# Kernel tuning notes

Hardware: AMD Instinct MI355X
Metric: run time of the kernel (lower is better)

Reference implementation:

```python
import jax, jax.numpy as jnp
import numpy as np

B, T, D, H, DFF = 64, 100, 1024, 16, 4096
HD = D // H
EPS = 1e-5


def _rope_tables(t_len, hd, dtype):
    # matches RotaryEmbedding: inv_freq over even dims, emb = cat([freqs, freqs])
    inv_freq = 1.0 / (10000.0 ** (jnp.arange(0, hd, 2, dtype=jnp.float32) / hd))
    t = jnp.arange(t_len, dtype=jnp.float32)
    freqs = jnp.einsum('i,j->ij', t, inv_freq)          # (T, hd/2)
    emb = jnp.concatenate([freqs, freqs], axis=-1)      # (T, hd)
    # apply_rope uses cos[..., ::2] / sin[..., ::2]
    cos = jnp.cos(emb)[:, ::2].astype(dtype)            # (T, hd/2)
    sin = jnp.sin(emb)[:, ::2].astype(dtype)
    return cos, sin


def _apply_rope(x, cos, sin):
    # x: (B, H, T, hd); cos/sin: (T, hd/2) broadcast over B,H
    x1 = x[..., ::2]
    x2 = x[..., 1::2]
    return jnp.concatenate([x1 * cos - x2 * sin, x1 * sin + x2 * cos], axis=-1)


def _layernorm(x, g, b):
    mu = jnp.mean(x, axis=-1, keepdims=True)
    var = jnp.mean(jnp.square(x - mu), axis=-1, keepdims=True)
    return (x - mu) * jax.lax.rsqrt(var + EPS) * g + b


def setup_inputs() -> dict:
    key = jax.random.key(0)
    ks = jax.random.split(key, 8)
    s = 0.02
    return {
        'tgt': jax.random.normal(ks[0], (B, T, D), dtype=jnp.float32),
        'Wqkv': jax.random.normal(ks[1], (3 * D, D), dtype=jnp.float32) * s,
        'bqkv': jnp.zeros((3 * D,), jnp.float32),
        'Wo': jax.random.normal(ks[2], (D, D), dtype=jnp.float32) * s,
        'bo': jnp.zeros((D,), jnp.float32),
        'W1': jax.random.normal(ks[3], (DFF, D), dtype=jnp.float32) * s,
        'b1': jnp.zeros((DFF,), jnp.float32),
        'W2': jax.random.normal(ks[4], (D, DFF), dtype=jnp.float32) * s,
        'b2': jnp.zeros((D,), jnp.float32),
        'g1': jnp.ones((D,), jnp.float32),
        'be1': jnp.zeros((D,), jnp.float32),
        'g2': jnp.ones((D,), jnp.float32),
        'be2': jnp.zeros((D,), jnp.float32),
        'tgt_mask': jnp.tril(jnp.ones((T, T), jnp.int32)),
    }


def reference(tgt, Wqkv, bqkv, Wo, bo, W1, b1, W2, b2, g1, be1, g2, be2, tgt_mask):
    dtype = tgt.dtype
    # QKV projection (torch Linear: x @ W.T + b)
    qkv = jnp.einsum('btd,ed->bte', tgt, Wqkv) + bqkv          # (B,T,3D)
    qkv = qkv.reshape(B, T, 3, H, HD).transpose(2, 0, 3, 1, 4)  # (3,B,H,T,hd)
    q, k, v = qkv[0], qkv[1], qkv[2]

    cos, sin = _rope_tables(T, HD, dtype)
    q = _apply_rope(q, cos, sin)
    k = _apply_rope(k, cos, sin)

    scale = 1.0 / np.sqrt(HD)
    scores = jnp.einsum('bhqd,bhkd->bhqk', q, k) * scale        # (B,H,T,T)
    scores = jnp.where(tgt_mask == 0, -jnp.inf, scores)
    attn = jax.nn.softmax(scores, axis=-1)
    ctx = jnp.einsum('bhqk,bhkd->bhqd', attn, v)                # (B,H,T,hd)
    ctx = ctx.transpose(0, 2, 1, 3).reshape(B, T, D)

    tgt2 = jnp.einsum('btd,ed->bte', ctx, Wo) + bo
    x = _layernorm(tgt + tgt2, g1, be1)

    h = jax.nn.relu(jnp.einsum('btd,fd->btf', x, W1) + b1)
    ff = jnp.einsum('btf,df->btd', h, W2) + b2
    out = _layernorm(x + ff, g2, be2)
    return out
```

## Files before the change

### kernel.cpp

```cpp
#include <hip/hip_runtime.h>
#include <math.h>

#define Bn   64
#define Tn   100
#define Tp   128
#define Dn   1024
#define Hn   16
#define HDn  64
#define DFFn 4096
#define EPSf 1e-5f

typedef unsigned short ushort_t;
typedef __attribute__((ext_vector_type(8))) __bf16 bf16x8;
typedef __attribute__((ext_vector_type(4))) float f32x4;

__device__ __forceinline__ float u2f(ushort_t u) {
    union { unsigned int i; float f; } v; v.i = ((unsigned int)u) << 16; return v.f;
}
__device__ __forceinline__ ushort_t f2bf(float f) {
    union { float f; unsigned int u; } v; v.f = f;
    unsigned int r = v.u + 0x7FFFu + ((v.u >> 16) & 1u);
    return (ushort_t)(r >> 16);
}

__device__ __forceinline__ void gload_lds16(const void* g, void* l) {
    __builtin_amdgcn_global_load_lds(
        (const __attribute__((address_space(1))) unsigned int*)g,
        (__attribute__((address_space(3))) unsigned int*)l,
        16, 0, 0);
}

#define VMWAIT_(n) asm volatile("s_waitcnt vmcnt(" #n ")" ::: "memory")
#define VMWAIT(n)  VMWAIT_(n)

struct ConvSeg { const float* src; ushort_t* dst; int n4; };
struct Conv5   { ConvSeg seg[5]; };

__global__ __launch_bounds__(256) void conv_bf16_multi(Conv5 cfg)
{
    int i = blockIdx.x * 256 + threadIdx.x;
    #pragma unroll
    for (int s = 0; s < 5; ++s) {
        const int n = cfg.seg[s].n4;
        if (i < n) {
            float4 v = ((const float4*)cfg.seg[s].src)[i];
            ushort4 o;
            o.x = f2bf(v.x); o.y = f2bf(v.y); o.z = f2bf(v.z); o.w = f2bf(v.w);
            ((ushort4*)cfg.seg[s].dst)[i] = o;
            return;
        }
        i -= n;
    }
}

#define GEMM_TILE_MAP(gx_, gy_, swz_)                                        \
    const int L  = blockIdx.x;                                               \
    int rowt, colt;                                                          \
    if (swz_) {                                                              \
        const int group = L / (8 * (gx_));                                   \
        int l = L - group * 8 * (gx_);                                       \
        const int rem = (gy_) - group * 8;                                   \
        if (rem >= 8) { rowt = group * 8 + (l & 7); colt = l >> 3; }         \
        else          { rowt = group * 8 + l % rem; colt = l / rem; }        \
    } else { rowt = L / (gx_); colt = L - rowt * (gx_); }

#define GEMM_KLOOP(A_, B_, K_)                                               \
    for (int k0 = 0; k0 < (K_); k0 += 64) {                                  \
        __syncthreads();                                                     \
        _Pragma("unroll")                                                    \
        for (int t = 0; t < 4; ++t) {                                        \
            const int idx = (wave * 4 + t) * 64 + lane;                      \
            const int row = idx >> 3;                                        \
            const int gc  = (idx & 7) ^ (row & 7);                           \
            gload_lds16((A_) + (size_t)(row0 + row) * (K_) + k0 + gc * 8,    \
                        &As[idx * 8]);                                       \
            gload_lds16((B_) + (size_t)(col0 + row) * (K_) + k0 + gc * 8,    \
                        &Bs[idx * 8]);                                       \
        }                                                                    \
        __syncthreads();                                                     \
        _Pragma("unroll")                                                    \
        for (int kh = 0; kh < 2; ++kh) {                                     \
            const int chunk = kh * 4 + g;                                    \
            bf16x8 af[4], bfr[4];                                            \
            _Pragma("unroll")                                                \
            for (int i = 0; i < 4; ++i) {                                    \
                const int ra = wrow + i * 16 + frow;                         \
                af[i]  = *(const bf16x8*)&As[ra * 64 + (chunk ^ (ra & 7)) * 8]; \
                const int rb = wcol + i * 16 + frow;                         \
                bfr[i] = *(const bf16x8*)&Bs[rb * 64 + (chunk ^ (rb & 7)) * 8]; \
            }                                                                \
            _Pragma("unroll")                                                \
            for (int i = 0; i < 4; ++i)                                      \
                _Pragma("unroll")                                            \
                for (int j = 0; j < 4; ++j)                                  \
                    acc[i][j] = __builtin_amdgcn_mfma_f32_16x16x32_bf16(     \
                        af[i], bfr[j], acc[i][j], 0, 0, 0);                  \
        }                                                                    \
    }

template<int BN, bool RELU, bool ADDRES, typename OutT>
__global__ __launch_bounds__(512, 2) void gemm256_bt(const ushort_t* __restrict__ A,
                                                     const ushort_t* __restrict__ Bm,
                                                     const float* __restrict__ bias,
                                                     const ushort_t* __restrict__ res,
                                                     OutT* __restrict__ C,
                                                     int M, int N, int K,
                                                     int gx, int swz)
{
    constexpr int JN = BN / 64;
    constexpr int NB = BN / 128;
    __shared__ __align__(16) ushort_t As[2][256 * 64];
    __shared__ __align__(16) ushort_t Bs[2][BN * 64];

    const int gy = M >> 8;
    GEMM_TILE_MAP(gx, gy, swz)

    const int tid  = threadIdx.x;
    const int lane = tid & 63;
    const int wave = tid >> 6;
    const int wm   = wave >> 2;
    const int wn   = wave & 3;
    const int row0 = rowt * 256;
    const int col0 = colt * BN;
    const int frow = lane & 15;
    const int g    = lane >> 4;

    auto stageA = [&](const ushort_t* src, int rowbase, ushort_t* lds) {
        #pragma unroll
        for (int i = 0; i < 2; ++i) {
            const int idx = i * 512 + tid;
            const int row = idx >> 3;
            const int gc  = (idx & 7) ^ (row & 7);
            gload_lds16(src + (size_t)(rowbase + row) * K + gc * 8, lds + idx * 8);
        }
    };
    auto stageB = [&](const ushort_t* src, int rowbase, ushort_t* lds) {
        #pragma unroll
        for (int i = 0; i < NB; ++i) {
            const int idx = i * 512 + tid;
            const int row = idx >> 3;
            const int gc  = (idx & 7) ^ (row & 7);
            gload_lds16(src + (size_t)(rowbase + row) * K + gc * 8, lds + idx * 8);
        }
    };

    f32x4 acc[8][JN] = {};

    const int NT = K >> 6;
    stageB(Bm,      col0,          &Bs[0][0]);
    stageB(Bm,      col0 + BN / 2, &Bs[0][(BN / 2) * 64]);
    stageA(A,       row0,          &As[0][0]);
    stageA(A,       row0 + 128,    &As[0][128 * 64]);
    stageB(Bm + 64, col0,          &Bs[1][0]);
    stageB(Bm + 64, col0 + BN / 2, &Bs[1][(BN / 2) * 64]);
    if constexpr (NB == 2) { VMWAIT(4); } else { VMWAIT(2); }
    __builtin_amdgcn_s_barrier();

    for (int t = 0; t < NT; ++t) {
        const int  buf = t & 1;
        const bool stA = (t + 1 < NT);
        const bool stB = (t + 2 < NT);

        if constexpr (BN == 128) {
            bf16x8 bfr[JN][2];
            #pragma unroll
            for (int j = 0; j < JN; ++j)
                #pragma unroll
                for (int kk = 0; kk < 2; ++kk) {
                    const int rb = wn * (BN / 4) + j * 16 + frow;
                    const int ch = kk * 4 + g;
                    bfr[j][kk] = *(const bf16x8*)&Bs[buf][rb * 64 + (ch ^ (rb & 7)) * 8];
                }
            bf16x8 af0[4][2];
            #pragma unroll
            for (int m = 0; m < 4; ++m)
                #pragma unroll
                for (int kk = 0; kk < 2; ++kk) {
                    const int ra = wm * 128 + m * 16 + frow;
                    const int ch = kk * 4 + g;
                    af0[m][kk] = *(const bf16x8*)&As[buf][ra * 64 + (ch ^ (ra & 7)) * 8];
                }
            if (stA) {
                stageA(A + (t + 1) * 64, row0,       &As[buf ^ 1][0]);
                stageA(A + (t + 1) * 64, row0 + 128, &As[buf ^ 1][128 * 64]);
            }
            __builtin_amdgcn_s_barrier();
            asm volatile("s_waitcnt lgkmcnt(0)" ::: "memory");
            __builtin_amdgcn_sched_barrier(0);
            __builtin_amdgcn_s_setprio(1);
            #pragma unroll
            for (int m = 0; m < 4; ++m)
                #pragma unroll
                for (int j = 0; j < JN; ++j)
                    #pragma unroll
                    for (int kk = 0; kk < 2; ++kk)
                        acc[m][j] = __builtin_amdgcn_mfma_f32_16x16x32_bf16(
                            af0[m][kk], bfr[j][kk], acc[m][j], 0, 0, 0);
            __builtin_amdgcn_s_setprio(0);
            __builtin_amdgcn_sched_barrier(0);
            __builtin_amdgcn_s_barrier();

            bf16x8 af1[4][2];
            #pragma unroll
            for (int m = 0; m < 4; ++m)
                #pragma unroll
                for (int kk = 0; kk < 2; ++kk) {
                    const int ra = wm * 128 + (4 + m) * 16 + frow;
                    const int ch = kk * 4 + g;
                    af1[m][kk] = *(const bf16x8*)&As[buf][ra * 64 + (ch ^ (ra & 7)) * 8];
                }
            if (stB) {
                stageB(Bm + (t + 2) * 64, col0,          &Bs[buf][0]);
                stageB(Bm + (t + 2) * 64, col0 + BN / 2, &Bs[buf][(BN / 2) * 64]);
            }
            __builtin_amdgcn_s_barrier();
            asm volatile("s_waitcnt lgkmcnt(0)" ::: "memory");
            __builtin_amdgcn_sched_barrier(0);
            __builtin_amdgcn_s_setprio(1);
            #pragma unroll
            for (int m = 0; m < 4; ++m)
                #pragma unroll
                for (int j = 0; j < JN; ++j)
                    #pragma unroll
                    for (int kk = 0; kk < 2; ++kk)
                        acc[4 + m][j] = __builtin_amdgcn_mfma_f32_16x16x32_bf16(
                            af1[m][kk], bfr[j][kk], acc[4 + m][j], 0, 0, 0);
            __builtin_amdgcn_s_setprio(0);
            __builtin_amdgcn_sched_barrier(0);
            if (stB)      { VMWAIT(2); }
            else if (stA) { VMWAIT(0); }
            __builtin_amdgcn_s_barrier();
        } else {
            bf16x8 bfr[JN][2];
            #pragma unroll
            for (int q = 0; q < 4; ++q) {
                bf16x8 af[2][2];
                #pragma unroll
                for (int ii = 0; ii < 2; ++ii)
                    #pragma unroll
                    for (int kk = 0; kk < 2; ++kk) {
                        const int ra = wm * 128 + (2 * q + ii) * 16 + frow;
                        const int ch = kk * 4 + g;
                        af[ii][kk] = *(const bf16x8*)&As[buf][ra * 64 + (ch ^ (ra & 7)) * 8];
                    }
                if (q == 0) {
                    #pragma unroll
                    for (int j = 0; j < JN; ++j)
                        #pragma unroll
                        for (int kk = 0; kk < 2; ++kk) {
                            const int rb = wn * (BN / 4) + j * 16 + frow;
                            const int ch = kk * 4 + g;
                            bfr[j][kk] = *(const bf16x8*)&Bs[buf][rb * 64 + (ch ^ (rb & 7)) * 8];
                        }
                }
                if (q == 0 && stA) stageA(A + (t + 1) * 64, row0,       &As[buf ^ 1][0]);
                if (q == 1 && stA) stageA(A + (t + 1) * 64, row0 + 128, &As[buf ^ 1][128 * 64]);
                if (q == 2 && stB) stageB(Bm + (t + 2) * 64, col0,          &Bs[buf][0]);
                if (q == 3 && stB) stageB(Bm + (t + 2) * 64, col0 + BN / 2, &Bs[buf][(BN / 2) * 64]);
                __builtin_amdgcn_s_barrier();
                asm volatile("s_waitcnt lgkmcnt(0)" ::: "memory");
                __builtin_amdgcn_sched_barrier(0);
                __builtin_amdgcn_s_setprio(1);
                #pragma unroll
                for (int ii = 0; ii < 2; ++ii)
                    #pragma unroll
                    for (int j = 0; j < JN; ++j)
                        #pragma unroll
                        for (int kk = 0; kk < 2; ++kk)
                            acc[2 * q + ii][j] = __builtin_amdgcn_mfma_f32_16x16x32_bf16(
                                af[ii][kk], bfr[j][kk], acc[2 * q + ii][j], 0, 0, 0);
                __builtin_amdgcn_s_setprio(0);
                __builtin_amdgcn_sched_barrier(0);
                if (q == 3) {
                    if (stB)      { VMWAIT(4); }
                    else if (stA) { VMWAIT(0); }
                }
                __builtin_amdgcn_s_barrier();
            }
        }
    }

    const int crow = (lane >> 4) * 4;
    const int ccol = lane & 15;
    #pragma unroll
    for (int i = 0; i < 8; ++i) {
        #pragma unroll
        for (int r = 0; r < 4; ++r) {
            const int row = row0 + wm * 128 + i * 16 + crow + r;
            #pragma unroll
            for (int j = 0; j < JN; ++j) {
                const int col = col0 + wn * (BN / 4) + j * 16 + ccol;
                float v = acc[i][j][r] + bias[col];
                if constexpr (ADDRES) v += u2f(res[(size_t)row * N + col]);
                if constexpr (RELU) v = fmaxf(v, 0.f);
                if constexpr (sizeof(OutT) == 2)
                    C[(size_t)row * N + col] = (OutT)f2bf(v);
                else
                    C[(size_t)row * N + col] = (OutT)v;
            }
        }
    }
}

__global__ __launch_bounds__(256) void gemm_qkv_rope(const ushort_t* __restrict__ A,
                                                     const ushort_t* __restrict__ Bm,
                                                     const float* __restrict__ bias,
                                                     ushort_t* __restrict__ q,
                                                     ushort_t* __restrict__ k,
                                                     ushort_t* __restrict__ vt)
{
    __shared__ __align__(16) ushort_t As[128 * 64];
    __shared__ __align__(16) ushort_t Bs[128 * 64];

    const int gy = 50, gx = 24;
    GEMM_TILE_MAP(gx, gy, 1)

    const int tid  = threadIdx.x;
    const int wave = tid >> 6;
    const int lane = tid & 63;
    const int row0 = rowt * 128;
    const int col0 = colt * 128;
    const int wrow = (wave >> 1) * 64;
    const int wcol = (wave & 1) * 64;
    const int frow = lane & 15;
    const int g    = lane >> 4;

    f32x4 acc[4][4] = {};
    GEMM_KLOOP(A, Bm, Dn)

    const int sec = col0 >> 10;

    __syncthreads();
    float2* tab = (float2*)As;
    if (sec != 2) {
        for (int e = tid; e < 2048; e += 256) {
            const int lr = e >> 4, f = e & 15;
            const int row = row0 + lr;
            const int b = row / Tn;
            const int t = row - b * Tn;
            float s, c;
            sincosf((float)t * exp2f(-0.83048202f * (float)f), &s, &c);
            tab[lr * 16 + f] = make_float2(c, s);
        }
    }
    __syncthreads();

    const int crow = (lane >> 4) * 4;
    const int ccol = lane & 15;

    if (sec == 2) {
        #pragma unroll
        for (int i = 0; i < 4; ++i) {
            #pragma unroll
            for (int r = 0; r < 4; ++r) {
                const int row = row0 + wrow + i * 16 + crow + r;
                const int b = row / Tn, t = row - b * Tn;
                #pragma unroll
                for (int j = 0; j < 4; ++j) {
                    const int colg = col0 + wcol + j * 16 + ccol;
                    const int hcol = colg & 1023;
                    const int h = hcol >> 6, d = hcol & 63;
                    const float v = acc[i][j][r] + bias[colg];
                    vt[((size_t)(b * Hn + h) * HDn + d) * Tp + t] = f2bf(v);
                }
            }
        }
    } else {
        ushort_t* dst = sec ? k : q;
        const int odd = ccol & 1;
        const int f0  = ccol >> 1;
        #pragma unroll
        for (int i = 0; i < 4; ++i) {
            #pragma unroll
            for (int r = 0; r < 4; ++r) {
                const int lr  = wrow + i * 16 + crow + r;
                const int row = row0 + lr;
                const int b = row / Tn, t = row - b * Tn;
                const float2 cs0 = tab[lr * 16 + f0];
                const float2 cs1 = tab[lr * 16 + 8 + f0];
                (void)t;
                #pragma unroll
                for (int j = 0; j < 4; ++j) {
                    const int colg = col0 + wcol + j * 16 + ccol;
                    const int hcol = colg & 1023;
                    const int h  = hcol >> 6;
                    const int dh = hcol & 63;
                    const int m  = dh >> 1;
                    const float val   = acc[i][j][r] + bias[colg];
                    const float other = __shfl_xor(val, 1);
                    const float sn = (j & 1) ? cs1.y : cs0.y;
                    const float cs = (j & 1) ? cs1.x : cs0.x;
                    const float x1 = odd ? other : val;
                    const float x2 = odd ? val : other;
                    const float o  = odd ? (x1 * sn + x2 * cs)
                                         : (x1 * cs - x2 * sn);
                    const int outcol = odd ? (m + 32) : m;
                    dst[((size_t)(b * Hn + h) * Tp + t) * HDn + outcol] = f2bf(o);
                }
            }
        }
    }
}

__global__ __launch_bounds__(256) void attn_mfma(const ushort_t* __restrict__ q,
                                                 const ushort_t* __restrict__ k,
                                                 const ushort_t* __restrict__ vt,
                                                 ushort_t* __restrict__ ctx)
{
    __shared__ __align__(16) ushort_t sm[24576];

    const int bh   = blockIdx.x;
    const int b    = bh >> 4, h = bh & 15;
    const int tid  = threadIdx.x;
    const int wave = tid >> 6;
    const int lane = tid & 63;
    const int c    = lane & 15;
    const int g    = lane >> 4;
    const int R0   = wave * 32;

    const ushort_t* qg = q  + (size_t)bh * Tp * HDn;
    const ushort_t* kg = k  + (size_t)bh * Tp * HDn;
    const ushort_t* vg = vt + (size_t)bh * HDn * Tp;
    for (int s = wave; s < 16; s += 4) {
        const int idx = s * 64 + lane;
        { const int row = idx >> 3, pc = idx & 7, gc = pc ^ (row & 7);
          gload_lds16(qg + row * 64 + gc * 8, &sm[idx * 8]);
          gload_lds16(kg + row * 64 + gc * 8, &sm[8192 + idx * 8]); }
        { const int row = idx >> 4, pc = idx & 15, gc = pc ^ (row & 15);
          gload_lds16(vg + row * 128 + gc * 8, &sm[16384 + idx * 8]); }
    }
    __syncthreads();

    f32x4 acc[2][8] = {};
    #pragma unroll
    for (int ks = 0; ks < 2; ++ks) {
        const int cb = ks * 4;
        bf16x8 aq[2];
        #pragma unroll
        for (int i = 0; i < 2; ++i) {
            const int row = R0 + i * 16 + c;
            const int ph  = (cb + g) ^ (row & 7);
            aq[i] = *(const bf16x8*)&sm[row * 64 + ph * 8];
        }
        #pragma unroll
        for (int j = 0; j < 8; ++j) {
            const int row = j * 16 + c;
            const int ph  = (cb + g) ^ (row & 7);
            const bf16x8 bk = *(const bf16x8*)&sm[8192 + row * 64 + ph * 8];
            acc[0][j] = __builtin_amdgcn_mfma_f32_16x16x32_bf16(aq[0], bk, acc[0][j], 0, 0, 0);
            acc[1][j] = __builtin_amdgcn_mfma_f32_16x16x32_bf16(aq[1], bk, acc[1][j], 0, 0, 0);
        }
    }
    __syncthreads();

    float linv[2][4];
    #pragma unroll
    for (int i = 0; i < 2; ++i) {
        #pragma unroll
        for (int r = 0; r < 4; ++r) {
            const int row = R0 + i * 16 + g * 4 + r;
            float sv[8], m = -1e30f;
            #pragma unroll
            for (int j = 0; j < 8; ++j) {
                const int col = j * 16 + c;
                const float s = acc[i][j][r] * 0.125f;
                sv[j] = (col <= row) ? s : -1e30f;
                m = fmaxf(m, sv[j]);
            }
            #pragma unroll
            for (int msk = 1; msk < 16; msk <<= 1) m = fmaxf(m, __shfl_xor(m, msk));
            float l = 0.f;
            #pragma unroll
            for (int j = 0; j < 8; ++j) {
                const int col = j * 16 + c;
                const float p = (col <= row) ? __expf(sv[j] - m) : 0.f;
                sv[j] = p; l += p;
            }
            #pragma unroll
            for (int msk = 1; msk < 16; msk <<= 1) l += __shfl_xor(l, msk);
            linv[i][r] = 1.f / l;
            #pragma unroll
            for (int j = 0; j < 8; ++j) {
                const int chunk = j * 2 + (c >> 3);
                const int ph    = chunk ^ (row & 15);
                sm[row * 128 + ph * 8 + (c & 7)] = f2bf(sv[j]);
            }
        }
    }
    __syncthreads();

    f32x4 acc2[2][4] = {};
    #pragma unroll
    for (int ks = 0; ks < 4; ++ks) {
        const int cb = ks * 4;
        bf16x8 ap[2];
        #pragma unroll
        for (int i = 0; i < 2; ++i) {
            const int row = R0 + i * 16 + c;
            const int ph  = (cb + g) ^ (row & 15);
            ap[i] = *(const bf16x8*)&sm[row * 128 + ph * 8];
        }
        #pragma unroll
        for (int n = 0; n < 4; ++n) {
            const int row = n * 16 + c;
            const int ph  = (cb + g) ^ (row & 15);
            const bf16x8 bv = *(const bf16x8*)&sm[16384 + row * 128 + ph * 8];
            acc2[0][n] = __builtin_amdgcn_mfma_f32_16x16x32_bf16(ap[0], bv, acc2[0][n], 0, 0, 0);
            acc2[1][n] = __builtin_amdgcn_mfma_f32_16x16x32_bf16(ap[1], bv, acc2[1][n], 0, 0, 0);
        }
    }

    #pragma unroll
    for (int i = 0; i < 2; ++i) {
        #pragma unroll
        for (int r = 0; r < 4; ++r) {
            const int row = R0 + i * 16 + g * 4 + r;
            if (row < Tn) {
                const float s = linv[i][r];
                #pragma unroll
                for (int n = 0; n < 4; ++n) {
                    const int col = n * 16 + c;
                    ctx[(size_t)(b * Tn + row) * Dn + h * HDn + col] =
                        f2bf(acc2[i][n][r] * s);
                }
            }
        }
    }
}

__global__ __launch_bounds__(256) void ln_single(const ushort_t* __restrict__ a,
                                                 const float* __restrict__ g,
                                                 const float* __restrict__ be,
                                                 ushort_t* __restrict__ out_bf)
{
    const int row = blockIdx.x;
    const int tid = threadIdx.x;
    __shared__ float red[256];
    const size_t base = (size_t)row * Dn;

    float vals[4];
    float s = 0.f;
    #pragma unroll
    for (int i = 0; i < 4; ++i) {
        const int c = tid + i * 256;
        vals[i] = u2f(a[base + c]);
        s += vals[i];
    }
    red[tid] = s;
    __syncthreads();
    for (int o = 128; o > 0; o >>= 1) {
        if (tid < o) red[tid] += red[tid + o];
        __syncthreads();
    }
    const float mu = red[0] * (1.f / Dn);
    __syncthreads();

    float vs = 0.f;
    #pragma unroll
    for (int i = 0; i < 4; ++i) { const float d = vals[i] - mu; vs += d * d; }
    red[tid] = vs;
    __syncthreads();
    for (int o = 128; o > 0; o >>= 1) {
        if (tid < o) red[tid] += red[tid + o];
        __syncthreads();
    }
    const float rstd = rsqrtf(red[0] * (1.f / Dn) + EPSf);

    #pragma unroll
    for (int i = 0; i < 4; ++i) {
        const int c = tid + i * 256;
        out_bf[base + c] = f2bf((vals[i] - mu) * rstd * g[c] + be[c]);
    }
}

__global__ __launch_bounds__(256) void add_ln2(const ushort_t* __restrict__ a,
                                               const ushort_t* __restrict__ r,
                                               const float* __restrict__ g,
                                               const float* __restrict__ be,
                                               float* __restrict__ out)
{
    const int row = blockIdx.x;
    const int tid = threadIdx.x;
    __shared__ float red[256];
    const size_t base = (size_t)row * Dn;

    float vals[4];
    float s = 0.f;
    #pragma unroll
    for (int i = 0; i < 4; ++i) {
        const int c = tid + i * 256;
        vals[i] = u2f(a[base + c]) + u2f(r[base + c]);
        s += vals[i];
    }
    red[tid] = s;
    __syncthreads();
    for (int o = 128; o > 0; o >>= 1) {
        if (tid < o) red[tid] += red[tid + o];
        __syncthreads();
    }
    const float mu = red[0] * (1.f / Dn);
    __syncthreads();

    float vs = 0.f;
    #pragma unroll
    for (int i = 0; i < 4; ++i) { const float d = vals[i] - mu; vs += d * d; }
    red[tid] = vs;
    __syncthreads();
    for (int o = 128; o > 0; o >>= 1) {
        if (tid < o) red[tid] += red[tid + o];
        __syncthreads();
    }
    const float rstd = rsqrtf(red[0] * (1.f / Dn) + EPSf);

    #pragma unroll
    for (int i = 0; i < 4; ++i) {
        const int c = tid + i * 256;
        out[base + c] = (vals[i] - mu) * rstd * g[c] + be[c];
    }
}

extern "C" void kernel_launch(void* const* d_in, const int* in_sizes, int n_in,
                              void* d_out, int out_size, void* d_ws, size_t ws_size,
                              hipStream_t stream)
{
    const float* tgt  = (const float*)d_in[0];
    const float* Wqkv = (const float*)d_in[1];
    const float* bqkv = (const float*)d_in[2];
    const float* Wo   = (const float*)d_in[3];
    const float* bo   = (const float*)d_in[4];
    const float* W1   = (const float*)d_in[5];
    const float* b1   = (const float*)d_in[6];
    const float* W2   = (const float*)d_in[7];
    const float* b2   = (const float*)d_in[8];
    const float* g1   = (const float*)d_in[9];
    const float* be1  = (const float*)d_in[10];
    const float* g2   = (const float*)d_in[11];
    const float* be2  = (const float*)d_in[12];
    float* out = (float*)d_out;
    (void)in_sizes; (void)n_in; (void)out_size; (void)ws_size;

    const int M = Bn * Tn;

    char* w = (char*)d_ws;
    ushort_t* tgt_bf  = (ushort_t*)(w);
    ushort_t* Wqkv_bf = (ushort_t*)(w + 13107200);
    ushort_t* Wo_bf   = (ushort_t*)(w + 19398656);
    ushort_t* W1_bf   = (ushort_t*)(w + 21495808);
    ushort_t* W2_bf   = (ushort_t*)(w + 29884416);

    ushort_t* qb    = (ushort_t*)(w + 38273024);
    ushort_t* kb    = (ushort_t*)(w + 55050240);
    ushort_t* vtb   = (ushort_t*)(w + 71827456);
    ushort_t* hbuf  = (ushort_t*)(w + 38273024);
    ushort_t* ctxb  = (ushort_t*)(w + 88604672);
    ushort_t* tgt2b = (ushort_t*)(w + 101711872);
    ushort_t* ffb   = (ushort_t*)(w + 101711872);
    ushort_t* x_bf  = (ushort_t*)(w + 114819072);

    Conv5 cfg;
    cfg.seg[0] = { tgt,  tgt_bf,  M * Dn / 4 };
    cfg.seg[1] = { Wqkv, Wqkv_bf, 3 * Dn * Dn / 4 };
    cfg.seg[2] = { Wo,   Wo_bf,   Dn * Dn / 4 };
    cfg.seg[3] = { W1,   W1_bf,   DFFn * Dn / 4 };
    cfg.seg[4] = { W2,   W2_bf,   Dn * DFFn / 4 };
    const int total4 = (M * Dn + 3 * Dn * Dn + Dn * Dn + 2 * DFFn * Dn) / 4;
    conv_bf16_multi<<<(total4 + 255) / 256, 256, 0, stream>>>(cfg);

    gemm_qkv_rope<<<1200, 256, 0, stream>>>(tgt_bf, Wqkv_bf, bqkv, qb, kb, vtb);
    attn_mfma<<<Bn * Hn, 256, 0, stream>>>(qb, kb, vtb, ctxb);
    gemm256_bt<128, false, true, ushort_t><<<(Dn / 128) * (M / 256), 512, 0, stream>>>(
        ctxb, Wo_bf, bo, tgt_bf, tgt2b, M, Dn, Dn, Dn / 128, 1);
    ln_single<<<M, 256, 0, stream>>>(tgt2b, g1, be1, x_bf);
    gemm256_bt<256, true, false, ushort_t><<<(M / 256) * (DFFn / 256), 512, 0, stream>>>(
        x_bf, W1_bf, b1, nullptr, hbuf, M, DFFn, Dn, DFFn / 256, 0);
    gemm256_bt<128, false, false, ushort_t><<<(Dn / 128) * (M / 256), 512, 0, stream>>>(
        hbuf, W2_bf, b2, nullptr, ffb, M, Dn, DFFn, Dn / 128, 1);
    add_ln2<<<M, 256, 0, stream>>>(x_bf, ffb, g2, be2, out);
}
```

Measured before the change: 423.1 us.

## Route QKV projection through tuned 256-row GEMM and split RoPE into separate kernel

Replaces the fused 128x128 QKV GEMM+RoPE kernel with the existing double-buffered 256x128 GEMM writing a plain bf16 QKV buffer, followed by a new per-(batch,head) kernel that applies RoPE and transposes V through LDS. The RoPE sin/cos table is now computed once by an extra block of the conversion kernel instead of per GEMM tile. This aims to use the faster GEMM mainloop and remove redundant sincos work, at the cost of an extra kernel launch and a full round trip of the QKV activations through memory.

```diff
diff --git a/kernel.cpp b/kernel.cpp
--- a/kernel.cpp
+++ b/kernel.cpp
@@ -34,10 +34,19 @@
 #define VMWAIT(n)  VMWAIT_(n)
 
 struct ConvSeg { const float* src; ushort_t* dst; int n4; };
-struct Conv5   { ConvSeg seg[5]; };
+struct Conv5   { ConvSeg seg[5]; float2* tab; };
 
 __global__ __launch_bounds__(256) void conv_bf16_multi(Conv5 cfg)
 {
+    if (blockIdx.x == gridDim.x - 1) {
+        for (int e = threadIdx.x; e < Tn * 16; e += 256) {
+            const int t = e >> 4, f = e & 15;
+            float s, c;
+            sincosf((float)t * exp2f(-0.83048202f * (float)f), &s, &c);
+            cfg.tab[e] = make_float2(c, s);
+        }
+        return;
+    }
     int i = blockIdx.x * 256 + threadIdx.x;
     #pragma unroll
     for (int s = 0; s < 5; ++s) {
@@ -63,40 +72,6 @@
         if (rem >= 8) { rowt = group * 8 + (l & 7); colt = l >> 3; }         \
         else          { rowt = group * 8 + l % rem; colt = l / rem; }        \
     } else { rowt = L / (gx_); colt = L - rowt * (gx_); }
-
-#define GEMM_KLOOP(A_, B_, K_)                                               \
-    for (int k0 = 0; k0 < (K_); k0 += 64) {                                  \
-        __syncthreads();                                                     \
-        _Pragma("unroll")                                                    \
-        for (int t = 0; t < 4; ++t) {                                        \
-            const int idx = (wave * 4 + t) * 64 + lane;                      \
-            const int row = idx >> 3;                                        \
-            const int gc  = (idx & 7) ^ (row & 7);                           \
-            gload_lds16((A_) + (size_t)(row0 + row) * (K_) + k0 + gc * 8,    \
-                        &As[idx * 8]);                                       \
-            gload_lds16((B_) + (size_t)(col0 + row) * (K_) + k0 + gc * 8,    \
-                        &Bs[idx * 8]);                                       \
-        }                                                                    \
-        __syncthreads();                                                     \
-        _Pragma("unroll")                                                    \
-        for (int kh = 0; kh < 2; ++kh) {                                     \
-            const int chunk = kh * 4 + g;                                    \
-            bf16x8 af[4], bfr[4];                                            \
-            _Pragma("unroll")                                                \
-            for (int i = 0; i < 4; ++i) {                                    \
-                const int ra = wrow + i * 16 + frow;                         \
-                af[i]  = *(const bf16x8*)&As[ra * 64 + (chunk ^ (ra & 7)) * 8]; \
-                const int rb = wcol + i * 16 + frow;                         \
-                bfr[i] = *(const bf16x8*)&Bs[rb * 64 + (chunk ^ (rb & 7)) * 8]; \
-            }                                                                \
-            _Pragma("unroll")                                                \
-            for (int i = 0; i < 4; ++i)                                      \
-                _Pragma("unroll")                                            \
-                for (int j = 0; j < 4; ++j)                                  \
-                    acc[i][j] = __builtin_amdgcn_mfma_f32_16x16x32_bf16(     \
-                        af[i], bfr[j], acc[i][j], 0, 0, 0);                  \
-        }                                                                    \
-    }
 
 template<int BN, bool RELU, bool ADDRES, typename OutT>
 __global__ __launch_bounds__(512, 2) void gemm256_bt(const ushort_t* __restrict__ A,
@@ -302,103 +277,51 @@
     }
 }
 
-__global__ __launch_bounds__(256) void gemm_qkv_rope(const ushort_t* __restrict__ A,
-                                                     const ushort_t* __restrict__ Bm,
-                                                     const float* __restrict__ bias,
-                                                     ushort_t* __restrict__ q,
-                                                     ushort_t* __restrict__ k,
-                                                     ushort_t* __restrict__ vt)
+__global__ __launch_bounds__(256) void rope_split(const ushort_t* __restrict__ qkv,
+                                                  const float2*  __restrict__ tab,
+                                                  ushort_t* __restrict__ q,
+                                                  ushort_t* __restrict__ k,
+                                                  ushort_t* __restrict__ vt)
 {
-    __shared__ __align__(16) ushort_t As[128 * 64];
-    __shared__ __align__(16) ushort_t Bs[128 * 64];
-
-    const int gy = 50, gx = 24;
-    GEMM_TILE_MAP(gx, gy, 1)
-
-    const int tid  = threadIdx.x;
-    const int wave = tid >> 6;
-    const int lane = tid & 63;
-    const int row0 = rowt * 128;
-    const int col0 = colt * 128;
-    const int wrow = (wave >> 1) * 64;
-    const int wcol = (wave & 1) * 64;
-    const int frow = lane & 15;
-    const int g    = lane >> 4;
-
-    f32x4 acc[4][4] = {};
-    GEMM_KLOOP(A, Bm, Dn)
-
-    const int sec = col0 >> 10;
-
-    __syncthreads();
-    float2* tab = (float2*)As;
-    if (sec != 2) {
-        for (int e = tid; e < 2048; e += 256) {
-            const int lr = e >> 4, f = e & 15;
-            const int row = row0 + lr;
-            const int b = row / Tn;
-            const int t = row - b * Tn;
-            float s, c;
-            sincosf((float)t * exp2f(-0.83048202f * (float)f), &s, &c);
-            tab[lr * 16 + f] = make_float2(c, s);
-        }
-    }
-    __syncthreads();
-
-    const int crow = (lane >> 4) * 4;
-    const int ccol = lane & 15;
-
-    if (sec == 2) {
-        #pragma unroll
-        for (int i = 0; i < 4; ++i) {
-            #pragma unroll
-            for (int r = 0; r < 4; ++r) {
-                const int row = row0 + wrow + i * 16 + crow + r;
-                const int b = row / Tn, t = row - b * Tn;
-                #pragma unroll
-                for (int j = 0; j < 4; ++j) {
-                    const int colg = col0 + wcol + j * 16 + ccol;
-                    const int hcol = colg & 1023;
-                    const int h = hcol >> 6, d = hcol & 63;
-                    const float v = acc[i][j][r] + bias[colg];
-                    vt[((size_t)(b * Hn + h) * HDn + d) * Tp + t] = f2bf(v);
-                }
-            }
-        }
-    } else {
-        ushort_t* dst = sec ? k : q;
-        const int odd = ccol & 1;
-        const int f0  = ccol >> 1;
-        #pragma unroll
-        for (int i = 0; i < 4; ++i) {
-            #pragma unroll
-            for (int r = 0; r < 4; ++r) {
-                const int lr  = wrow + i * 16 + crow + r;
-                const int row = row0 + lr;
-                const int b = row / Tn, t = row - b * Tn;
-                const float2 cs0 = tab[lr * 16 + f0];
-                const float2 cs1 = tab[lr * 16 + 8 + f0];
-                (void)t;
-                #pragma unroll
-                for (int j = 0; j < 4; ++j) {
-                    const int colg = col0 + wcol + j * 16 + ccol;
-                    const int hcol = colg & 1023;
-                    const int h  = hcol >> 6;
-                    const int dh = hcol & 63;
-                    const int m  = dh >> 1;
-                    const float val   = acc[i][j][r] + bias[colg];
-                    const float other = __shfl_xor(val, 1);
-                    const float sn = (j & 1) ? cs1.y : cs0.y;
-                    const float cs = (j & 1) ? cs1.x : cs0.x;
-                    const float x1 = odd ? other : val;
-                    const float x2 = odd ? val : other;
-                    const float o  = odd ? (x1 * sn + x2 * cs)
-                                         : (x1 * cs - x2 * sn);
-                    const int outcol = odd ? (m + 32) : m;
-                    dst[((size_t)(b * Hn + h) * Tp + t) * HDn + outcol] = f2bf(o);
-                }
-            }
-        }
+    __shared__ ushort_t vls[64 * 130];
+
+    const int bh  = blockIdx.x;
+    const int b   = bh >> 4, h = bh & 15;
+    const int tid = threadIdx.x;
+    const size_t rowbase = (size_t)b * Tn * (3 * Dn) + h * HDn;
+
+    const ushort_t* vsrc = qkv + rowbase + 2 * Dn;
+    for (int idx = tid; idx < Tn * 64; idx += 256) {
+        const int t = idx >> 6, d = idx & 63;
+        vls[d * 130 + t] = vsrc[(size_t)t * (3 * Dn) + d];
+    }
+
+    #pragma unroll
+    for (int s = 0; s < 2; ++s) {
+        const ushort_t* src = qkv + rowbase + s * Dn;
+        ushort_t* dst = (s ? k : q) + (size_t)bh * Tp * HDn;
+        for (int idx = tid; idx < Tn * 32; idx += 256) {
+            const int t = idx >> 5, p = idx & 31;
+            const unsigned int xi =
+                *(const unsigned int*)&src[(size_t)t * (3 * Dn) + 2 * p];
+            const float x1 = u2f((ushort_t)(xi & 0xffffu));
+            const float x2 = u2f((ushort_t)(xi >> 16));
+            const float2 cs = tab[t * 16 + (p & 15)];
+            dst[t * 64 + p]      = f2bf(x1 * cs.x - x2 * cs.y);
+            dst[t * 64 + 32 + p] = f2bf(x1 * cs.y + x2 * cs.x);
+        }
+    }
+
+    __syncthreads();
+
+    ushort_t* vdst = vt + (size_t)bh * HDn * Tp;
+    for (int idx = tid; idx < 64 * 64; idx += 256) {
+        const int d  = idx >> 6;
+        const int tt = (idx & 63) * 2;
+        ushort2 o;
+        o.x = (tt     < Tn) ? vls[d * 130 + tt]     : (ushort_t)0;
+        o.y = (tt + 1 < Tn) ? vls[d * 130 + tt + 1] : (ushort_t)0;
+        *(ushort2*)&vdst[d * Tp + tt] = o;
     }
 }
 
@@ -652,10 +575,12 @@
     ushort_t* kb    = (ushort_t*)(w + 55050240);
     ushort_t* vtb   = (ushort_t*)(w + 71827456);
     ushort_t* hbuf  = (ushort_t*)(w + 38273024);
+    ushort_t* qkvb  = (ushort_t*)(w + 88604672);
     ushort_t* ctxb  = (ushort_t*)(w + 88604672);
     ushort_t* tgt2b = (ushort_t*)(w + 101711872);
     ushort_t* ffb   = (ushort_t*)(w + 101711872);
     ushort_t* x_bf  = (ushort_t*)(w + 114819072);
+    float2*   ropetab = (float2*)(w + 127926272);
 
     Conv5 cfg;
     cfg.seg[0] = { tgt,  tgt_bf,  M * Dn / 4 };
@@ -663,10 +588,13 @@
     cfg.seg[2] = { Wo,   Wo_bf,   Dn * Dn / 4 };
     cfg.seg[3] = { W1,   W1_bf,   DFFn * Dn / 4 };
     cfg.seg[4] = { W2,   W2_bf,   Dn * DFFn / 4 };
+    cfg.tab    = ropetab;
     const int total4 = (M * Dn + 3 * Dn * Dn + Dn * Dn + 2 * DFFn * Dn) / 4;
-    conv_bf16_multi<<<(total4 + 255) / 256, 256, 0, stream>>>(cfg);
-
-    gemm_qkv_rope<<<1200, 256, 0, stream>>>(tgt_bf, Wqkv_bf, bqkv, qb, kb, vtb);
+    conv_bf16_multi<<<(total4 + 255) / 256 + 1, 256, 0, stream>>>(cfg);
+
+    gemm256_bt<128, false, false, ushort_t><<<600, 512, 0, stream>>>(
+        tgt_bf, Wqkv_bf, bqkv, nullptr, qkvb, M, 3 * Dn, Dn, 24, 1);
+    rope_split<<<Bn * Hn, 256, 0, stream>>>(qkvb, ropetab, qb, kb, vtb);
     attn_mfma<<<Bn * Hn, 256, 0, stream>>>(qb, kb, vtb, ctxb);
     gemm256_bt<128, false, true, ushort_t><<<(Dn / 128) * (M / 256), 512, 0, stream>>>(
         ctxb, Wo_bf, bo, tgt_bf, tgt2b, M, Dn, Dn, Dn / 128, 1);
```

Result: no change. 419.0 us (-1.0%).
